# Performance work log

Hardware: AMD Instinct MI355X
Metric: run time of the kernel (lower is better)

## Reference

```python
import jax, jax.numpy as jnp
import numpy as np
from jax import lax

B, N, C_IN, C_OUT = 8, 8192, 64, 128
NUM_SAMPLES, K = 2048, 32
EPS = 1e-5


def _bn(x, g, b, m, v):
    # inference-mode BatchNorm1d over channel axis 1; x: [G, C, L]
    scale = g / jnp.sqrt(v + EPS)
    return (x - m[None, :, None]) * scale[None, :, None] + b[None, :, None]


def _conv1x1(x, w):
    # kernel_size=1 Conv1d (no bias); x: [G, Cin, L], w: [Cout, Cin]
    return jnp.einsum('gck,oc->gok', x, w)


def _res_block(x, w1, g1, b1, m1, v1, w2, g2, b2, m2, v2):
    # conv-bn-relu -> conv-bn, residual add, relu (residual_factor=1.0)
    y = jax.nn.relu(_bn(_conv1x1(x, w1), g1, b1, m1, v1))
    y = _bn(_conv1x1(y, w2), g2, b2, m2, v2)
    return jax.nn.relu(y + x)


def _fps(xyz, num_samples):
    # farthest point sampling; xyz: [B,N,3] -> indices [B,S]
    b, n, _ = xyz.shape

    def step(carry, _):
        dists, last_idx = carry
        last_pt = jnp.take_along_axis(xyz, last_idx[:, None, None], axis=1)  # [B,1,3]
        d = jnp.sum((xyz - last_pt) ** 2, axis=-1)  # [B,N]
        dists = jnp.minimum(dists, d)
        nxt = jnp.argmax(dists, axis=-1).astype(jnp.int32)
        return (dists, nxt), last_idx

    init = (jnp.full((b, n), 1e10, xyz.dtype), jnp.zeros((b,), jnp.int32))
    _, idxs = lax.scan(step, init, None, length=num_samples)
    return jnp.transpose(idxs)  # [B,S]


def setup_inputs():
    key = jax.random.key(0)
    ks = jax.random.split(key, 40)
    xyz = jax.random.uniform(ks[0], (B, N, 3), jnp.float32)
    feat = jax.random.normal(ks[1], (B, N, C_IN), jnp.float32)

    def conv_w(k, o, c):
        return jax.random.normal(k, (o, c), jnp.float32) * (1.0 / np.sqrt(c).astype(np.float32))

    def bn_params(k, c):
        k1, k2, k3, k4 = jax.random.split(k, 4)
        return (1.0 + 0.1 * jax.random.normal(k1, (c,), jnp.float32),
                0.1 * jax.random.normal(k2, (c,), jnp.float32),
                0.1 * jax.random.normal(k3, (c,), jnp.float32),
                jax.random.uniform(k4, (c,), jnp.float32, 0.5, 1.5))

    inp = {'xyz': xyz, 'feat': feat}
    inp['te_w'] = conv_w(ks[2], C_OUT, 2 * C_IN)
    inp['te_g'], inp['te_b'], inp['te_m'], inp['te_v'] = bn_params(ks[3], C_OUT)
    for name, base in (('pre', 4), ('pos', 14)):
        inp[name + '_w1'] = jnp.stack([conv_w(ks[base + i], C_OUT, C_OUT) for i in range(2)])
        inp[name + '_w2'] = jnp.stack([conv_w(ks[base + 2 + i], C_OUT, C_OUT) for i in range(2)])
        bn1 = [bn_params(ks[base + 4 + i], C_OUT) for i in range(2)]
        bn2 = [bn_params(ks[base + 6 + i], C_OUT) for i in range(2)]
        for j, s in enumerate(('g', 'b', 'm', 'v')):
            inp[f'{name}_{s}1'] = jnp.stack([bn1[i][j] for i in range(2)])
            inp[f'{name}_{s}2'] = jnp.stack([bn2[i][j] for i in range(2)])
    return inp


def reference(xyz, feat, te_w, te_g, te_b, te_m, te_v,
              pre_w1, pre_w2, pre_g1, pre_b1, pre_m1, pre_v1, pre_g2, pre_b2, pre_m2, pre_v2,
              pos_w1, pos_w2, pos_g1, pos_b1, pos_m1, pos_v1, pos_g2, pos_b2, pos_m2, pos_v2):
    bsz = xyz.shape[0]
    # --- LocalGrouper: FPS centers + kNN grouping + concat center feat ---
    fps_idx = _fps(xyz, NUM_SAMPLES)                                    # [B,S]
    new_xyz = jnp.take_along_axis(xyz, fps_idx[..., None], axis=1)      # [B,S,3]
    ctr_feat = jnp.take_along_axis(feat, fps_idx[..., None], axis=1)    # [B,S,C]
    d2 = jnp.sum((new_xyz[:, :, None, :] - xyz[:, None, :, :]) ** 2, axis=-1)  # [B,S,N]
    _, knn_idx = lax.top_k(-d2, K)                                      # [B,S,K]
    grouped = feat[jnp.arange(bsz)[:, None, None], knn_idx]             # [B,S,K,C]
    ctr = jnp.broadcast_to(ctr_feat[:, :, None, :], grouped.shape)
    nf = jnp.concatenate([grouped, ctr], axis=-1)                       # [B,S,K,2C]
    # --- permute/view -> [B*S, 2C, K] ---
    x = nf.transpose(0, 1, 3, 2).reshape(bsz * NUM_SAMPLES, 2 * C_IN, K)
    x = jax.nn.relu(_bn(_conv1x1(x, te_w), te_g, te_b, te_m, te_v))     # [G,OUT,K]
    for i in range(2):
        x = _res_block(x, pre_w1[i], pre_g1[i], pre_b1[i], pre_m1[i], pre_v1[i],
                       pre_w2[i], pre_g2[i], pre_b2[i], pre_m2[i], pre_v2[i])
    x = jnp.max(x, axis=-1)                                             # adaptive_max_pool1d(.,1)
    x = x.reshape(bsz, NUM_SAMPLES, C_OUT).transpose(0, 2, 1)           # [B,OUT,S]
    for i in range(2):
        x = _res_block(x, pos_w1[i], pos_g1[i], pos_b1[i], pos_m1[i], pos_v1[i],
                       pos_w2[i], pos_g2[i], pos_b2[i], pos_m2[i], pos_v2[i])
    return new_xyz, x
```

## Files before the change

kernel.cpp:

```cpp
#include <hip/hip_runtime.h>

typedef unsigned short u16;
typedef unsigned int   u32;
typedef unsigned long long u64;

#define B_    8
#define N_    8192
#define CIN   64
#define COUT  128
#define NS    2048
#define K_    32
#define LDSPAD 136

typedef __attribute__((ext_vector_type(8))) short short8;
typedef __attribute__((ext_vector_type(4))) float f32x4;

#define MFMA16(a,b,c) __builtin_amdgcn_mfma_f32_16x16x32_bf16(a,b,c,0,0,0)

__device__ __forceinline__ u16 f2bf(float f){
  u32 u = __float_as_uint(f);
  return (u16)((u + 0x7FFFu + ((u >> 16) & 1u)) >> 16);
}
__device__ __forceinline__ float bf2f(u16 h){ u32 u = ((u32)h) << 16; return __uint_as_float(u); }
__device__ __forceinline__ u32 pack2bf(float lo, float hi){ return (u32)f2bf(lo) | ((u32)f2bf(hi) << 16); }

__global__ void wcvt_kernel(const float* __restrict__ s, u16* __restrict__ d, int n){
  int i = blockIdx.x * 256 + threadIdx.x;
  if (i < n) d[i] = f2bf(s[i]);
}

struct BnPtrs { const float* g[9]; const float* b[9]; const float* m[9]; const float* v[9]; };

__global__ void bn_pre_kernel(BnPtrs p, float* __restrict__ bns){
  int set = blockIdx.x, c = threadIdx.x;
  float sc = p.g[set][c] / sqrtf(p.v[set][c] + 1e-5f);
  bns[set*256 + c]       = sc;
  bns[set*256 + 128 + c] = p.b[set][c] - p.m[set][c] * sc;
}

#define DPP_UMAX(x, ctrl) { \
  u32 o = (u32)__builtin_amdgcn_update_dpp((int)(x), (int)(x), ctrl, 0xf, 0xf, false); \
  x = (o > x) ? o : x; }

__device__ __forceinline__ u32 wave_umax63(u32 x){
  DPP_UMAX(x, 0x111)
  DPP_UMAX(x, 0x112)
  DPP_UMAX(x, 0x114)
  DPP_UMAX(x, 0x118)
  DPP_UMAX(x, 0x142)
  DPP_UMAX(x, 0x143)
  return (u32)__builtin_amdgcn_readlane((int)x, 63);
}

#define FPS_STEP4(j) { \
  f32x4 xv = PX4[j*512 + t]; \
  f32x4 yv = PY4[j*512 + t]; \
  f32x4 zv = PZ4[j*512 + t]; \
  FPS_ONE(j,0) FPS_ONE(j,1) FPS_ONE(j,2) FPS_ONE(j,3) }

#define FPS_ONE(j,i) { \
  float dx = xv[i] - lx; \
  float dy = yv[i] - ly; \
  float dz = zv[i] - lz; \
  float t0 = dx*dx; \
  float t1 = dy*dy; \
  float t2 = dz*dz; \
  float dd = (t0 + t1) + t2;   \
  float nd = fminf(D##j##i, dd); \
  D##j##i = nd; \
  u32 nb = __float_as_uint(nd); \
  tb##j = (nb > tb##j) ? nb : tb##j; }

#define FPS_KMIN(j,i) \
  kk = (__float_as_uint(D##j##i) == wmax && (4*j+i) < kk) ? (4*j+i) : kk;

__global__ __launch_bounds__(512) void fps_kernel(const float* __restrict__ xyz, int* __restrict__ fps_idx){
  #pragma clang fp contract(off)
  const int b = blockIdx.x;
  const int t = threadIdx.x;
  const int lane = t & 63, wv = t >> 6;
  const float* xb = xyz + (size_t)b * N_ * 3;
  __shared__ __align__(16) f32x4 PX4[4*512], PY4[4*512], PZ4[4*512];
  __shared__ u64  kArr[2][8];
  __shared__ float xA[2][8], yA[2][8], zA[2][8];
  const int base = t * 16;
  #pragma unroll
  for (int j = 0; j < 4; ++j){
    f32x4 xv, yv, zv;
    #pragma unroll
    for (int i = 0; i < 4; ++i){
      const int p = base + 4*j + i;
      xv[i] = xb[p*3 + 0];
      yv[i] = xb[p*3 + 1];
      zv[i] = xb[p*3 + 2];
    }
    PX4[j*512 + t] = xv; PY4[j*512 + t] = yv; PZ4[j*512 + t] = zv;
  }
  if (t == 0) fps_idx[b*NS] = 0;
  __syncthreads();
  float D00=1e10f,D01=1e10f,D02=1e10f,D03=1e10f;
  float D10=1e10f,D11=1e10f,D12=1e10f,D13=1e10f;
  float D20=1e10f,D21=1e10f,D22=1e10f,D23=1e10f;
  float D30=1e10f,D31=1e10f,D32=1e10f,D33=1e10f;
  const float* PXs = (const float*)PX4;
  const float* PYs = (const float*)PY4;
  const float* PZs = (const float*)PZ4;
  float lx = PXs[0], ly = PYs[0], lz = PZs[0];
  for (int s = 0; s < NS - 1; ++s){
    u32 tb0 = 0, tb1 = 0, tb2 = 0, tb3 = 0;
    FPS_STEP4(0) FPS_STEP4(1) FPS_STEP4(2) FPS_STEP4(3)
    u32 ta = (tb0 > tb1) ? tb0 : tb1;
    u32 tc = (tb2 > tb3) ? tb2 : tb3;
    u32 tbm = (ta > tc) ? ta : tc;
    const u32 wmax = wave_umax63(tbm);
    const u64 mask = __ballot(tbm == wmax);
    const int fl = __ffsll((long long)mask) - 1;
    const int sl = s & 1;
    if (lane == fl){
      int kk = 64;
      FPS_KMIN(0,0) FPS_KMIN(0,1) FPS_KMIN(0,2) FPS_KMIN(0,3)
      FPS_KMIN(1,0) FPS_KMIN(1,1) FPS_KMIN(1,2) FPS_KMIN(1,3)
      FPS_KMIN(2,0) FPS_KMIN(2,1) FPS_KMIN(2,2) FPS_KMIN(2,3)
      FPS_KMIN(3,0) FPS_KMIN(3,1) FPS_KMIN(3,2) FPS_KMIN(3,3)
      const int pi = base + kk;
      kArr[sl][wv] = ((u64)wmax << 13) | (u64)(8191 - pi);
      const int li = ((kk >> 2)*512 + t)*4 + (kk & 3);
      xA[sl][wv] = PXs[li]; yA[sl][wv] = PYs[li]; zA[sl][wv] = PZs[li];
    }
    __syncthreads();
    u64 win = kArr[sl][0];
    float cx = xA[sl][0], cy = yA[sl][0], cz = zA[sl][0];
    #pragma unroll
    for (int w = 1; w < 8; ++w){
      u64 o = kArr[sl][w];
      float ox = xA[sl][w], oy = yA[sl][w], oz = zA[sl][w];
      bool c = o > win;
      win = c ? o : win; cx = c ? ox : cx; cy = c ? oy : cy; cz = c ? oz : cz;
    }
    lx = cx; ly = cy; lz = cz;
    if (t == 0) fps_idx[b*NS + s + 1] = 8191 - (int)(win & 0x1FFFull);
  }
}

__global__ __launch_bounds__(256) void knn_kernel(const float* __restrict__ xyz, const int* __restrict__ fps_idx,
                                                  int* __restrict__ knn, float* __restrict__ out_xyz){
  #pragma clang fp contract(off)
  const int wid = threadIdx.x >> 6, lane = threadIdx.x & 63;
  const int cg = blockIdx.x * 4 + wid;
  const int b = cg >> 11;
  const float* xb = xyz + (size_t)b * N_ * 3;
  const int ci = fps_idx[cg] & (N_ - 1);
  const float cx = xb[ci*3], cy = xb[ci*3+1], cz = xb[ci*3+2];
  if (lane < 3) out_xyz[cg*3 + lane] = xb[ci*3 + lane];

  float rd = __uint_as_float(0x7F800000u); int ri = 0x7FFFFFFF;
  float r31d = rd; int r31i = ri;
  for (int c = 0; c < N_/64; ++c){
    const int pid = c*64 + lane;
    float dx = xb[pid*3]   - cx;
    float dy = xb[pid*3+1] - cy;
    float dz = xb[pid*3+2] - cz;
    float t0 = dx*dx, t1 = dy*dy, t2 = dz*dz;
    float d2 = (t0 + t1) + t2;
    u64 m = __ballot((d2 < r31d) || (d2 == r31d && pid < r31i));
    while (m){
      int l = __ffsll((long long)m) - 1; m &= m - 1;
      float v = __shfl(d2, l); int vi = c*64 + l;
      if (!((v < r31d) || (v == r31d && vi < r31i))) continue;
      bool lt = (rd < v) || (rd == v && ri < vi);
      int pos = __popcll(__ballot(lt));
      float prd = __shfl_up(rd, 1); int pri = __shfl_up(ri, 1);
      if (lane == pos){ rd = v; ri = vi; }
      else if (lane > pos){ rd = prd; ri = pri; }
      r31d = __shfl(rd, 31); r31i = __shfl(ri, 31);
    }
  }
  if (lane < K_) knn[(size_t)cg * K_ + lane] = ri;
}

__device__ __forceinline__ void zero_acc(f32x4 acc[8][2]){
  #pragma unroll
  for (int mt = 0; mt < 8; ++mt)
    #pragma unroll
    for (int nt = 0; nt < 2; ++nt){
      acc[mt][nt][0] = 0.f; acc[mt][nt][1] = 0.f; acc[mt][nt][2] = 0.f; acc[mt][nt][3] = 0.f;
    }
}

__device__ __forceinline__ void conv_step(const u16* __restrict__ W, const u16* __restrict__ Xw,
                                          int q, int l15, f32x4 acc[8][2]){
  #pragma unroll
  for (int kk = 0; kk < 4; ++kk){
    short8 b0 = *(const short8*)(Xw + l15*LDSPAD + kk*32 + q*8);
    short8 b1 = *(const short8*)(Xw + (16 + l15)*LDSPAD + kk*32 + q*8);
    #pragma unroll
    for (int mt = 0; mt < 8; ++mt){
      short8 a = *(const short8*)(W + (size_t)(mt*16 + l15)*COUT + kk*32 + q*8);
      acc[mt][0] = MFMA16(a, b0, acc[mt][0]);
      acc[mt][1] = MFMA16(a, b1, acc[mt][1]);
    }
  }
}

__device__ __forceinline__ void res_block(const u16* __restrict__ W1, const u16* __restrict__ W2,
    const float* __restrict__ bn1, const float* __restrict__ bn2,
    u16* __restrict__ Xw, int q, int l15, u32 resid[8][2][2], f32x4 acc[8][2], bool writeback){
  zero_acc(acc);
  conv_step(W1, Xw, q, l15, acc);
  #pragma unroll
  for (int mt = 0; mt < 8; ++mt){
    f32x4 sc = *(const f32x4*)(bn1 + mt*16 + q*4);
    f32x4 bi = *(const f32x4*)(bn1 + 128 + mt*16 + q*4);
    #pragma unroll
    for (int nt = 0; nt < 2; ++nt){
      float y0 = fmaxf(fmaf(acc[mt][nt][0], sc[0], bi[0]), 0.f);
      float y1 = fmaxf(fmaf(acc[mt][nt][1], sc[1], bi[1]), 0.f);
      float y2 = fmaxf(fmaf(acc[mt][nt][2], sc[2], bi[2]), 0.f);
      float y3 = fmaxf(fmaf(acc[mt][nt][3], sc[3], bi[3]), 0.f);
      *(uint2*)(Xw + (nt*16 + l15)*LDSPAD + mt*16 + q*4) = make_uint2(pack2bf(y0,y1), pack2bf(y2,y3));
    }
  }
  __syncthreads();
  zero_acc(acc);
  conv_step(W2, Xw, q, l15, acc);
  #pragma unroll
  for (int mt = 0; mt < 8; ++mt){
    f32x4 sc = *(const f32x4*)(bn2 + mt*16 + q*4);
    f32x4 bi = *(const f32x4*)(bn2 + 128 + mt*16 + q*4);
    #pragma unroll
    for (int nt = 0; nt < 2; ++nt){
      float r0 = bf2f((u16)(resid[mt][nt][0] & 0xFFFFu));
      float r1 = bf2f((u16)(resid[mt][nt][0] >> 16));
      float r2 = bf2f((u16)(resid[mt][nt][1] & 0xFFFFu));
      float r3 = bf2f((u16)(resid[mt][nt][1] >> 16));
      float y0 = fmaxf(fmaf(acc[mt][nt][0], sc[0], bi[0]) + r0, 0.f);
      float y1 = fmaxf(fmaf(acc[mt][nt][1], sc[1], bi[1]) + r1, 0.f);
      float y2 = fmaxf(fmaf(acc[mt][nt][2], sc[2], bi[2]) + r2, 0.f);
      float y3 = fmaxf(fmaf(acc[mt][nt][3], sc[3], bi[3]) + r3, 0.f);
      acc[mt][nt][0] = y0; acc[mt][nt][1] = y1; acc[mt][nt][2] = y2; acc[mt][nt][3] = y3;
      if (writeback){
        u32 p0 = pack2bf(y0,y1), p1 = pack2bf(y2,y3);
        resid[mt][nt][0] = p0; resid[mt][nt][1] = p1;
        *(uint2*)(Xw + (nt*16 + l15)*LDSPAD + mt*16 + q*4) = make_uint2(p0, p1);
      }
    }
  }
  if (writeback) __syncthreads();
}

__global__ __launch_bounds__(256) void mid_kernel(const float* __restrict__ feat,
    const u16* __restrict__ te_w, const u16* __restrict__ pre_w1, const u16* __restrict__ pre_w2,
    const float* __restrict__ bns, const int* __restrict__ fps_idx, const int* __restrict__ knn,
    u16* __restrict__ x_mid){
  __shared__ __align__(16) u16 X[4][32*LDSPAD];
  __shared__ __align__(16) float scr[4][128];
  const int wid = threadIdx.x >> 6, lane = threadIdx.x & 63;
  const int q = lane >> 4, l15 = lane & 15;
  const int g = blockIdx.x*4 + wid;
  const int b = g >> 11;
  const float* fb = feat + (size_t)b * N_ * CIN;
  u16* Xw = X[wid];

  const int ctr = fps_idx[g] & (N_ - 1);
  const int* kg = knn + (size_t)g * K_;
  #pragma unroll
  for (int it = 0; it < 4; ++it){
    int lidx = it*64 + lane;
    int col = lidx >> 3, kq = lidx & 7;
    int nb = kg[col] & (N_ - 1);
    f32x4 a0 = *(const f32x4*)(fb + (size_t)nb*CIN + kq*8);
    f32x4 a1 = *(const f32x4*)(fb + (size_t)nb*CIN + kq*8 + 4);
    *(uint2*)(Xw + col*LDSPAD + kq*8)     = make_uint2(pack2bf(a0[0],a0[1]), pack2bf(a0[2],a0[3]));
    *(uint2*)(Xw + col*LDSPAD + kq*8 + 4) = make_uint2(pack2bf(a1[0],a1[1]), pack2bf(a1[2],a1[3]));
    f32x4 c0 = *(const f32x4*)(fb + (size_t)ctr*CIN + kq*8);
    f32x4 c1 = *(const f32x4*)(fb + (size_t)ctr*CIN + kq*8 + 4);
    *(uint2*)(Xw + col*LDSPAD + 64 + kq*8)     = make_uint2(pack2bf(c0[0],c0[1]), pack2bf(c0[2],c0[3]));
    *(uint2*)(Xw + col*LDSPAD + 64 + kq*8 + 4) = make_uint2(pack2bf(c1[0],c1[1]), pack2bf(c1[2],c1[3]));
  }
  __syncthreads();

  f32x4 acc[8][2];
  u32 resid[8][2][2];
  zero_acc(acc);
  conv_step(te_w, Xw, q, l15, acc);
  #pragma unroll
  for (int mt = 0; mt < 8; ++mt){
    f32x4 sc = *(const f32x4*)(bns + mt*16 + q*4);
    f32x4 bi = *(const f32x4*)(bns + 128 + mt*16 + q*4);
    #pragma unroll
    for (int nt = 0; nt < 2; ++nt){
      float y0 = fmaxf(fmaf(acc[mt][nt][0], sc[0], bi[0]), 0.f);
      float y1 = fmaxf(fmaf(acc[mt][nt][1], sc[1], bi[1]), 0.f);
      float y2 = fmaxf(fmaf(acc[mt][nt][2], sc[2], bi[2]), 0.f);
      float y3 = fmaxf(fmaf(acc[mt][nt][3], sc[3], bi[3]), 0.f);
      u32 p0 = pack2bf(y0,y1), p1 = pack2bf(y2,y3);
      resid[mt][nt][0] = p0; resid[mt][nt][1] = p1;
      *(uint2*)(Xw + (nt*16 + l15)*LDSPAD + mt*16 + q*4) = make_uint2(p0, p1);
    }
  }
  __syncthreads();

  res_block(pre_w1,             pre_w2,             bns + 256, bns + 512,  Xw, q, l15, resid, acc, true);
  res_block(pre_w1 + COUT*COUT, pre_w2 + COUT*COUT, bns + 768, bns + 1024, Xw, q, l15, resid, acc, false);

  float mx[8][4];
  #pragma unroll
  for (int mt = 0; mt < 8; ++mt)
    #pragma unroll
    for (int r = 0; r < 4; ++r){
      float m0 = fmaxf(acc[mt][0][r], acc[mt][1][r]);
      #pragma unroll
      for (int off = 1; off < 16; off <<= 1) m0 = fmaxf(m0, __shfl_xor(m0, off));
      mx[mt][r] = m0;
    }
  if (l15 == 0){
    #pragma unroll
    for (int mt = 0; mt < 8; ++mt){
      f32x4 vv; vv[0] = mx[mt][0]; vv[1] = mx[mt][1]; vv[2] = mx[mt][2]; vv[3] = mx[mt][3];
      *(f32x4*)(scr[wid] + mt*16 + q*4) = vv;
    }
  }
  __syncthreads();
  float v0 = scr[wid][lane*2], v1 = scr[wid][lane*2 + 1];
  *(u32*)(x_mid + (size_t)g*COUT + lane*2) = pack2bf(v0, v1);
}

__global__ __launch_bounds__(256) void pos_kernel(const u16* __restrict__ x_mid,
    const u16* __restrict__ pos_w1, const u16* __restrict__ pos_w2,
    const float* __restrict__ bns, float* __restrict__ out_x){
  __shared__ __align__(16) u16 X[4][32*LDSPAD];
  const int wid = threadIdx.x >> 6, lane = threadIdx.x & 63;
  const int q = lane >> 4, l15 = lane & 15;
  const int g = blockIdx.x*4 + wid;
  const int gc0 = g * 32;
  const int b = gc0 >> 11, s0 = gc0 & 2047;
  u16* Xw = X[wid];
  #pragma unroll
  for (int it = 0; it < 8; ++it){
    int lidx = it*64 + lane;
    int col = lidx >> 4, kq = lidx & 15;
    uint4 v = *(const uint4*)(x_mid + (size_t)(gc0 + col)*COUT + kq*8);
    *(uint4*)(Xw + col*LDSPAD + kq*8) = v;
  }
  __syncthreads();
  u32 resid[8][2][2];
  #pragma unroll
  for (int mt = 0; mt < 8; ++mt)
    #pragma unroll
    for (int nt = 0; nt < 2; ++nt){
      uint2 rr = *(const uint2*)(Xw + (nt*16 + l15)*LDSPAD + mt*16 + q*4);
      resid[mt][nt][0] = rr.x; resid[mt][nt][1] = rr.y;
    }
  f32x4 acc[8][2];
  res_block(pos_w1,             pos_w2,             bns + 1280, bns + 1536, Xw, q, l15, resid, acc, true);
  res_block(pos_w1 + COUT*COUT, pos_w2 + COUT*COUT, bns + 1792, bns + 2048, Xw, q, l15, resid, acc, false);
  #pragma unroll
  for (int mt = 0; mt < 8; ++mt)
    #pragma unroll
    for (int nt = 0; nt < 2; ++nt)
      #pragma unroll
      for (int r = 0; r < 4; ++r){
        int row = mt*16 + q*4 + r;
        int colx = s0 + nt*16 + l15;
        out_x[(size_t)(b*COUT + row)*NS + colx] = acc[mt][nt][r];
      }
}

extern "C" void kernel_launch(void* const* d_in, const int* in_sizes, int n_in,
                              void* d_out, int out_size, void* d_ws, size_t ws_size,
                              hipStream_t stream){
  (void)in_sizes; (void)n_in; (void)out_size; (void)ws_size;
  const float* xyz    = (const float*)d_in[0];
  const float* feat   = (const float*)d_in[1];

  char* ws = (char*)d_ws;
  float* bns     = (float*)ws;
  u16*   wbf     = (u16*)(ws + 16384);
  int*   fps_idx = (int*)(ws + 16384 + 294912);
  int*   knn     = (int*)(ws + 16384 + 294912 + 65536);
  u16*   x_mid   = (u16*)(ws + 16384 + 294912 + 65536 + 2097152);
  float* out_xyz = (float*)d_out;
  float* out_x   = (float*)d_out + B_*NS*3;

  u16* te_w   = wbf;
  u16* pre_w1 = wbf + 16384;
  u16* pre_w2 = wbf + 49152;
  u16* pos_w1 = wbf + 81920;
  u16* pos_w2 = wbf + 114688;
  wcvt_kernel<<<64,  256, 0, stream>>>((const float*)d_in[2],  te_w,   16384);
  wcvt_kernel<<<128, 256, 0, stream>>>((const float*)d_in[7],  pre_w1, 32768);
  wcvt_kernel<<<128, 256, 0, stream>>>((const float*)d_in[8],  pre_w2, 32768);
  wcvt_kernel<<<128, 256, 0, stream>>>((const float*)d_in[17], pos_w1, 32768);
  wcvt_kernel<<<128, 256, 0, stream>>>((const float*)d_in[18], pos_w2, 32768);

  BnPtrs bp;
  const int gi[9] = {3, 9, 10, 9, 10, 19, 20, 19, 20};
  const int bbi[9]= {4, 11,12, 11,12, 21, 22, 21, 22};
  const int mi[9] = {5, 13,14, 13,14, 23, 24, 23, 24};
  const int vi[9] = {6, 15,16, 15,16, 25, 26, 25, 26};
  const int of[9] = {0, 0, 0, 128,128, 0, 0, 128,128};
  for (int k = 0; k < 9; ++k){
    bp.g[k] = (const float*)d_in[gi[k]]  + of[k];
    bp.b[k] = (const float*)d_in[bbi[k]] + of[k];
    bp.m[k] = (const float*)d_in[mi[k]]  + of[k];
    bp.v[k] = (const float*)d_in[vi[k]]  + of[k];
  }

  bn_pre_kernel<<<9, 128, 0, stream>>>(bp, bns);
  fps_kernel<<<B_, 512, 0, stream>>>(xyz, fps_idx);
  knn_kernel<<<(B_*NS)/4, 256, 0, stream>>>(xyz, fps_idx, knn, out_xyz);
  mid_kernel<<<(B_*NS)/4, 256, 0, stream>>>(feat, te_w, pre_w1, pre_w2, bns, fps_idx, knn, x_mid);
  pos_kernel<<<(B_*NS/K_)/4, 256, 0, stream>>>(x_mid, pos_w1, pos_w2, bns, out_x);
}
```

Before: 2.965 ms.

## Split FPS across four cooperating blocks per batch with global-memory flag exchange

Farthest point sampling now runs on four blocks per batch, each owning a quarter of the points (4 per thread instead of 16). After each step's in-block reduction, each block publishes its winner to a per-step flag slot in global memory and spin-waits on the other three blocks' slots, then takes the global argmax. The aim is to cut the serial per-step work, since the old version had only 8 blocks doing 16 points per thread. The cost is a cross-block round trip through L2 every step, and correctness depends on all 32 blocks being co-resident. The flag buffer reuses the x_mid workspace and is cleared by an extra kernel.

```diff
diff --git a/kernel.cpp b/kernel.cpp
--- a/kernel.cpp
+++ b/kernel.cpp
@@ -12,6 +12,10 @@
 #define K_    32
 #define LDSPAD 136
 
+#define FPS_NBLK 4
+#define FPS_PPB  (N_/FPS_NBLK)
+#define FPS_PPT  (FPS_PPB/512)
+
 typedef __attribute__((ext_vector_type(8))) short short8;
 typedef __attribute__((ext_vector_type(4))) float f32x4;
 
@@ -27,6 +31,11 @@
 __global__ void wcvt_kernel(const float* __restrict__ s, u16* __restrict__ d, int n){
   int i = blockIdx.x * 256 + threadIdx.x;
   if (i < n) d[i] = f2bf(s[i]);
+}
+
+__global__ void fps_flags_clear_kernel(uint4* __restrict__ p, int n){
+  int i = blockIdx.x * 256 + threadIdx.x;
+  if (i < n) p[i] = make_uint4(0u, 0u, 0u, 0u);
 }
 
 struct BnPtrs { const float* g[9]; const float* b[9]; const float* m[9]; const float* v[9]; };
@@ -52,93 +61,91 @@
   return (u32)__builtin_amdgcn_readlane((int)x, 63);
 }
 
-#define FPS_STEP4(j) { \
-  f32x4 xv = PX4[j*512 + t]; \
-  f32x4 yv = PY4[j*512 + t]; \
-  f32x4 zv = PZ4[j*512 + t]; \
-  FPS_ONE(j,0) FPS_ONE(j,1) FPS_ONE(j,2) FPS_ONE(j,3) }
-
-#define FPS_ONE(j,i) { \
-  float dx = xv[i] - lx; \
-  float dy = yv[i] - ly; \
-  float dz = zv[i] - lz; \
-  float t0 = dx*dx; \
-  float t1 = dy*dy; \
-  float t2 = dz*dz; \
-  float dd = (t0 + t1) + t2;   \
-  float nd = fminf(D##j##i, dd); \
-  D##j##i = nd; \
-  u32 nb = __float_as_uint(nd); \
-  tb##j = (nb > tb##j) ? nb : tb##j; }
-
-#define FPS_KMIN(j,i) \
-  kk = (__float_as_uint(D##j##i) == wmax && (4*j+i) < kk) ? (4*j+i) : kk;
-
-__global__ __launch_bounds__(512) void fps_kernel(const float* __restrict__ xyz, int* __restrict__ fps_idx){
+__global__ __launch_bounds__(512) void fps_kernel(const float* __restrict__ xyz,
+                                                  int* __restrict__ fps_idx,
+                                                  u64* __restrict__ flags){
   #pragma clang fp contract(off)
-  const int b = blockIdx.x;
-  const int t = threadIdx.x;
+  const int bq = blockIdx.x;
+  const int b  = bq & 7;
+  const int q  = bq >> 3;
+  const int t  = threadIdx.x;
   const int lane = t & 63, wv = t >> 6;
   const float* xb = xyz + (size_t)b * N_ * 3;
-  __shared__ __align__(16) f32x4 PX4[4*512], PY4[4*512], PZ4[4*512];
-  __shared__ u64  kArr[2][8];
-  __shared__ float xA[2][8], yA[2][8], zA[2][8];
-  const int base = t * 16;
-  #pragma unroll
-  for (int j = 0; j < 4; ++j){
-    f32x4 xv, yv, zv;
+  __shared__ __align__(16) float PX[N_], PY[N_], PZ[N_];
+  __shared__ u64 kArr[2][8];
+  #pragma unroll
+  for (int i = 0; i < 16; ++i){
+    int p = t*16 + i;
+    PX[p] = xb[p*3 + 0];
+    PY[p] = xb[p*3 + 1];
+    PZ[p] = xb[p*3 + 2];
+  }
+  if (q == 0 && t == 0) fps_idx[b*NS] = 0;
+  __syncthreads();
+
+  const int base = q*FPS_PPB + t*4;
+  const f32x4 px = *(const f32x4*)(PX + base);
+  const f32x4 py = *(const f32x4*)(PY + base);
+  const f32x4 pz = *(const f32x4*)(PZ + base);
+  f32x4 D = {1e10f, 1e10f, 1e10f, 1e10f};
+  float lx = PX[0], ly = PY[0], lz = PZ[0];
+
+  u64* myflag = flags + ((size_t)(b*FPS_NBLK + q)) * NS;
+  u64* nf0 = flags + ((size_t)(b*FPS_NBLK + ((q+1)&3))) * NS;
+  u64* nf1 = flags + ((size_t)(b*FPS_NBLK + ((q+2)&3))) * NS;
+  u64* nf2 = flags + ((size_t)(b*FPS_NBLK + ((q+3)&3))) * NS;
+
+  for (int s = 0; s < NS - 1; ++s){
+    u32 tb = 0;
     #pragma unroll
     for (int i = 0; i < 4; ++i){
-      const int p = base + 4*j + i;
-      xv[i] = xb[p*3 + 0];
-      yv[i] = xb[p*3 + 1];
-      zv[i] = xb[p*3 + 2];
-    }
-    PX4[j*512 + t] = xv; PY4[j*512 + t] = yv; PZ4[j*512 + t] = zv;
-  }
-  if (t == 0) fps_idx[b*NS] = 0;
-  __syncthreads();
-  float D00=1e10f,D01=1e10f,D02=1e10f,D03=1e10f;
-  float D10=1e10f,D11=1e10f,D12=1e10f,D13=1e10f;
-  float D20=1e10f,D21=1e10f,D22=1e10f,D23=1e10f;
-  float D30=1e10f,D31=1e10f,D32=1e10f,D33=1e10f;
-  const float* PXs = (const float*)PX4;
-  const float* PYs = (const float*)PY4;
-  const float* PZs = (const float*)PZ4;
-  float lx = PXs[0], ly = PYs[0], lz = PZs[0];
-  for (int s = 0; s < NS - 1; ++s){
-    u32 tb0 = 0, tb1 = 0, tb2 = 0, tb3 = 0;
-    FPS_STEP4(0) FPS_STEP4(1) FPS_STEP4(2) FPS_STEP4(3)
-    u32 ta = (tb0 > tb1) ? tb0 : tb1;
-    u32 tc = (tb2 > tb3) ? tb2 : tb3;
-    u32 tbm = (ta > tc) ? ta : tc;
-    const u32 wmax = wave_umax63(tbm);
-    const u64 mask = __ballot(tbm == wmax);
+      float dx = px[i] - lx;
+      float dy = py[i] - ly;
+      float dz = pz[i] - lz;
+      float t0 = dx*dx;
+      float t1 = dy*dy;
+      float t2 = dz*dz;
+      float dd = (t0 + t1) + t2;
+      float nd = fminf(D[i], dd);
+      D[i] = nd;
+      u32 nb = __float_as_uint(nd);
+      tb = (nb > tb) ? nb : tb;
+    }
+    const u32 wmax = wave_umax63(tb);
+    const u64 mask = __ballot(tb == wmax);
     const int fl = __ffsll((long long)mask) - 1;
     const int sl = s & 1;
     if (lane == fl){
-      int kk = 64;
-      FPS_KMIN(0,0) FPS_KMIN(0,1) FPS_KMIN(0,2) FPS_KMIN(0,3)
-      FPS_KMIN(1,0) FPS_KMIN(1,1) FPS_KMIN(1,2) FPS_KMIN(1,3)
-      FPS_KMIN(2,0) FPS_KMIN(2,1) FPS_KMIN(2,2) FPS_KMIN(2,3)
-      FPS_KMIN(3,0) FPS_KMIN(3,1) FPS_KMIN(3,2) FPS_KMIN(3,3)
+      int kk = 3;
+      kk = (__float_as_uint(D[2]) == wmax) ? 2 : kk;
+      kk = (__float_as_uint(D[1]) == wmax) ? 1 : kk;
+      kk = (__float_as_uint(D[0]) == wmax) ? 0 : kk;
       const int pi = base + kk;
-      kArr[sl][wv] = ((u64)wmax << 13) | (u64)(8191 - pi);
-      const int li = ((kk >> 2)*512 + t)*4 + (kk & 3);
-      xA[sl][wv] = PXs[li]; yA[sl][wv] = PYs[li]; zA[sl][wv] = PZs[li];
-    }
+      kArr[sl][wv] = (1ull << 63) | ((u64)wmax << 13) | (u64)(8191 - pi);
+    }
+    u64 k0 = __hip_atomic_load(nf0 + s, __ATOMIC_RELAXED, __HIP_MEMORY_SCOPE_AGENT);
+    u64 k1 = __hip_atomic_load(nf1 + s, __ATOMIC_RELAXED, __HIP_MEMORY_SCOPE_AGENT);
+    u64 k2 = __hip_atomic_load(nf2 + s, __ATOMIC_RELAXED, __HIP_MEMORY_SCOPE_AGENT);
     __syncthreads();
     u64 win = kArr[sl][0];
-    float cx = xA[sl][0], cy = yA[sl][0], cz = zA[sl][0];
     #pragma unroll
     for (int w = 1; w < 8; ++w){
       u64 o = kArr[sl][w];
-      float ox = xA[sl][w], oy = yA[sl][w], oz = zA[sl][w];
-      bool c = o > win;
-      win = c ? o : win; cx = c ? ox : cx; cy = c ? oy : cy; cz = c ? oz : cz;
-    }
-    lx = cx; ly = cy; lz = cz;
-    if (t == 0) fps_idx[b*NS + s + 1] = 8191 - (int)(win & 0x1FFFull);
+      win = (o > win) ? o : win;
+    }
+    if (lane == 0)
+      __hip_atomic_store(myflag + s, win, __ATOMIC_RELAXED, __HIP_MEMORY_SCOPE_AGENT);
+    while (!((k0 & k1 & k2) >> 63)){
+      if (!(k0 >> 63)) k0 = __hip_atomic_load(nf0 + s, __ATOMIC_RELAXED, __HIP_MEMORY_SCOPE_AGENT);
+      if (!(k1 >> 63)) k1 = __hip_atomic_load(nf1 + s, __ATOMIC_RELAXED, __HIP_MEMORY_SCOPE_AGENT);
+      if (!(k2 >> 63)) k2 = __hip_atomic_load(nf2 + s, __ATOMIC_RELAXED, __HIP_MEMORY_SCOPE_AGENT);
+    }
+    win = (k0 > win) ? k0 : win;
+    win = (k1 > win) ? k1 : win;
+    win = (k2 > win) ? k2 : win;
+    const int pi = 8191 - (int)(win & 0x1FFFull);
+    lx = PX[pi]; ly = PY[pi]; lz = PZ[pi];
+    if (q == 0 && t == 0) fps_idx[b*NS + s + 1] = pi;
   }
 }
 
@@ -379,6 +386,7 @@
   int*   fps_idx = (int*)(ws + 16384 + 294912);
   int*   knn     = (int*)(ws + 16384 + 294912 + 65536);
   u16*   x_mid   = (u16*)(ws + 16384 + 294912 + 65536 + 2097152);
+  u64*   fflags  = (u64*)x_mid;
   float* out_xyz = (float*)d_out;
   float* out_x   = (float*)d_out + B_*NS*3;
 
@@ -392,6 +400,7 @@
   wcvt_kernel<<<128, 256, 0, stream>>>((const float*)d_in[8],  pre_w2, 32768);
   wcvt_kernel<<<128, 256, 0, stream>>>((const float*)d_in[17], pos_w1, 32768);
   wcvt_kernel<<<128, 256, 0, stream>>>((const float*)d_in[18], pos_w2, 32768);
+  fps_flags_clear_kernel<<<128, 256, 0, stream>>>((uint4*)fflags, (B_*FPS_NBLK*NS*8)/16);
 
   BnPtrs bp;
   const int gi[9] = {3, 9, 10, 9, 10, 19, 20, 19, 20};
@@ -407,7 +416,7 @@
   }
 
   bn_pre_kernel<<<9, 128, 0, stream>>>(bp, bns);
-  fps_kernel<<<B_, 512, 0, stream>>>(xyz, fps_idx);
+  fps_kernel<<<B_*FPS_NBLK, 512, 0, stream>>>(xyz, fps_idx, fflags);
   knn_kernel<<<(B_*NS)/4, 256, 0, stream>>>(xyz, fps_idx, knn, out_xyz);
   mid_kernel<<<(B_*NS)/4, 256, 0, stream>>>(feat, te_w, pre_w1, pre_w2, bns, fps_idx, knn, x_mid);
   pos_kernel<<<(B_*NS/K_)/4, 256, 0, stream>>>(x_mid, pos_w1, pos_w2, bns, out_x);
```

Result: slower. 3.463 ms (+16.8%).

## Fuse FPS, KNN, mid and pos stages into one persistent streaming megakernel

Applied to the files above, without the earlier changes.

Merges the FPS, KNN, grouped-conv mid stage and pos stage into a single launch. Blocks are dispatched by index: the FPS blocks publish each sampled index with release stores, and the KNN/mid waves spin-wait on those entries so neighbour search and convolution overlap the serial FPS loop. The pos waves wait on per-group done flags. KNN indices now stay in registers and are passed by shuffle instead of going through global memory. This depends on the FPS blocks being scheduled first and making progress alongside the spinning blocks, and it raises LDS and register use to a 512-thread block with a shared union.

```diff
diff --git a/kernel.cpp b/kernel.cpp
--- a/kernel.cpp
+++ b/kernel.cpp
@@ -29,6 +29,11 @@
   if (i < n) d[i] = f2bf(s[i]);
 }
 
+__global__ void clear_kernel(int* __restrict__ fps_idx, u32* __restrict__ done){
+  int i = blockIdx.x * 256 + threadIdx.x;
+  if (i < B_*NS){ fps_idx[i] = -1; done[i] = 0u; }
+}
+
 struct BnPtrs { const float* g[9]; const float* b[9]; const float* m[9]; const float* v[9]; };
 
 __global__ void bn_pre_kernel(BnPtrs p, float* __restrict__ bns){
@@ -37,6 +42,22 @@
   bns[set*256 + c]       = sc;
   bns[set*256 + 128 + c] = p.b[set][c] - p.m[set][c] * sc;
 }
+
+struct ShFps {
+  __align__(16) f32x4 PX4[4*512];
+  __align__(16) f32x4 PY4[4*512];
+  __align__(16) f32x4 PZ4[4*512];
+  u64  kArr[2][8];
+  float xA[2][8], yA[2][8], zA[2][8];
+};
+struct ShMid {
+  __align__(16) u16 X[8][32*LDSPAD];
+  __align__(16) float scr[8][128];
+};
+struct ShPos {
+  __align__(16) u16 X[8][32*LDSPAD];
+};
+union ShAll { ShFps f; ShMid m; ShPos p; };
 
 #define DPP_UMAX(x, ctrl) { \
   u32 o = (u32)__builtin_amdgcn_update_dpp((int)(x), (int)(x), ctrl, 0xf, 0xf, false); \
@@ -74,15 +95,12 @@
 #define FPS_KMIN(j,i) \
   kk = (__float_as_uint(D##j##i) == wmax && (4*j+i) < kk) ? (4*j+i) : kk;
 
-__global__ __launch_bounds__(512) void fps_kernel(const float* __restrict__ xyz, int* __restrict__ fps_idx){
+__device__ void fps_path(const float* __restrict__ xyz, int* __restrict__ fps_idx,
+                         ShFps& S, int b, int t){
   #pragma clang fp contract(off)
-  const int b = blockIdx.x;
-  const int t = threadIdx.x;
   const int lane = t & 63, wv = t >> 6;
   const float* xb = xyz + (size_t)b * N_ * 3;
-  __shared__ __align__(16) f32x4 PX4[4*512], PY4[4*512], PZ4[4*512];
-  __shared__ u64  kArr[2][8];
-  __shared__ float xA[2][8], yA[2][8], zA[2][8];
+  f32x4* PX4 = S.PX4; f32x4* PY4 = S.PY4; f32x4* PZ4 = S.PZ4;
   const int base = t * 16;
   #pragma unroll
   for (int j = 0; j < 4; ++j){
@@ -96,7 +114,8 @@
     }
     PX4[j*512 + t] = xv; PY4[j*512 + t] = yv; PZ4[j*512 + t] = zv;
   }
-  if (t == 0) fps_idx[b*NS] = 0;
+  if (t == 0)
+    __hip_atomic_store(fps_idx + b*NS, 0, __ATOMIC_RELEASE, __HIP_MEMORY_SCOPE_AGENT);
   __syncthreads();
   float D00=1e10f,D01=1e10f,D02=1e10f,D03=1e10f;
   float D10=1e10f,D11=1e10f,D12=1e10f,D13=1e10f;
@@ -123,35 +142,115 @@
       FPS_KMIN(2,0) FPS_KMIN(2,1) FPS_KMIN(2,2) FPS_KMIN(2,3)
       FPS_KMIN(3,0) FPS_KMIN(3,1) FPS_KMIN(3,2) FPS_KMIN(3,3)
       const int pi = base + kk;
-      kArr[sl][wv] = ((u64)wmax << 13) | (u64)(8191 - pi);
+      S.kArr[sl][wv] = ((u64)wmax << 13) | (u64)(8191 - pi);
       const int li = ((kk >> 2)*512 + t)*4 + (kk & 3);
-      xA[sl][wv] = PXs[li]; yA[sl][wv] = PYs[li]; zA[sl][wv] = PZs[li];
+      S.xA[sl][wv] = PXs[li]; S.yA[sl][wv] = PYs[li]; S.zA[sl][wv] = PZs[li];
     }
     __syncthreads();
-    u64 win = kArr[sl][0];
-    float cx = xA[sl][0], cy = yA[sl][0], cz = zA[sl][0];
+    u64 win = S.kArr[sl][0];
+    float cx = S.xA[sl][0], cy = S.yA[sl][0], cz = S.zA[sl][0];
     #pragma unroll
     for (int w = 1; w < 8; ++w){
-      u64 o = kArr[sl][w];
-      float ox = xA[sl][w], oy = yA[sl][w], oz = zA[sl][w];
+      u64 o = S.kArr[sl][w];
+      float ox = S.xA[sl][w], oy = S.yA[sl][w], oz = S.zA[sl][w];
       bool c = o > win;
       win = c ? o : win; cx = c ? ox : cx; cy = c ? oy : cy; cz = c ? oz : cz;
     }
     lx = cx; ly = cy; lz = cz;
-    if (t == 0) fps_idx[b*NS + s + 1] = 8191 - (int)(win & 0x1FFFull);
-  }
-}
-
-__global__ __launch_bounds__(256) void knn_kernel(const float* __restrict__ xyz, const int* __restrict__ fps_idx,
-                                                  int* __restrict__ knn, float* __restrict__ out_xyz){
+    if (t == 0)
+      __hip_atomic_store(fps_idx + b*NS + s + 1, 8191 - (int)(win & 0x1FFFull),
+                         __ATOMIC_RELEASE, __HIP_MEMORY_SCOPE_AGENT);
+  }
+}
+
+__device__ __forceinline__ void zero_acc(f32x4 acc[8][2]){
+  #pragma unroll
+  for (int mt = 0; mt < 8; ++mt)
+    #pragma unroll
+    for (int nt = 0; nt < 2; ++nt){
+      acc[mt][nt][0] = 0.f; acc[mt][nt][1] = 0.f; acc[mt][nt][2] = 0.f; acc[mt][nt][3] = 0.f;
+    }
+}
+
+__device__ __forceinline__ void conv_step(const u16* __restrict__ W, const u16* __restrict__ Xw,
+                                          int q, int l15, f32x4 acc[8][2]){
+  #pragma unroll
+  for (int kk = 0; kk < 4; ++kk){
+    short8 b0 = *(const short8*)(Xw + l15*LDSPAD + kk*32 + q*8);
+    short8 b1 = *(const short8*)(Xw + (16 + l15)*LDSPAD + kk*32 + q*8);
+    #pragma unroll
+    for (int mt = 0; mt < 8; ++mt){
+      short8 a = *(const short8*)(W + (size_t)(mt*16 + l15)*COUT + kk*32 + q*8);
+      acc[mt][0] = MFMA16(a, b0, acc[mt][0]);
+      acc[mt][1] = MFMA16(a, b1, acc[mt][1]);
+    }
+  }
+}
+
+__device__ __forceinline__ void res_block(const u16* __restrict__ W1, const u16* __restrict__ W2,
+    const float* __restrict__ bn1, const float* __restrict__ bn2,
+    u16* __restrict__ Xw, int q, int l15, u32 resid[8][2][2], f32x4 acc[8][2], bool writeback){
+  zero_acc(acc);
+  conv_step(W1, Xw, q, l15, acc);
+  #pragma unroll
+  for (int mt = 0; mt < 8; ++mt){
+    f32x4 sc = *(const f32x4*)(bn1 + mt*16 + q*4);
+    f32x4 bi = *(const f32x4*)(bn1 + 128 + mt*16 + q*4);
+    #pragma unroll
+    for (int nt = 0; nt < 2; ++nt){
+      float y0 = fmaxf(fmaf(acc[mt][nt][0], sc[0], bi[0]), 0.f);
+      float y1 = fmaxf(fmaf(acc[mt][nt][1], sc[1], bi[1]), 0.f);
+      float y2 = fmaxf(fmaf(acc[mt][nt][2], sc[2], bi[2]), 0.f);
+      float y3 = fmaxf(fmaf(acc[mt][nt][3], sc[3], bi[3]), 0.f);
+      *(uint2*)(Xw + (nt*16 + l15)*LDSPAD + mt*16 + q*4) = make_uint2(pack2bf(y0,y1), pack2bf(y2,y3));
+    }
+  }
+  __syncthreads();
+  zero_acc(acc);
+  conv_step(W2, Xw, q, l15, acc);
+  #pragma unroll
+  for (int mt = 0; mt < 8; ++mt){
+    f32x4 sc = *(const f32x4*)(bn2 + mt*16 + q*4);
+    f32x4 bi = *(const f32x4*)(bn2 + 128 + mt*16 + q*4);
+    #pragma unroll
+    for (int nt = 0; nt < 2; ++nt){
+      float r0 = bf2f((u16)(resid[mt][nt][0] & 0xFFFFu));
+      float r1 = bf2f((u16)(resid[mt][nt][0] >> 16));
+      float r2 = bf2f((u16)(resid[mt][nt][1] & 0xFFFFu));
+      float r3 = bf2f((u16)(resid[mt][nt][1] >> 16));
+      float y0 = fmaxf(fmaf(acc[mt][nt][0], sc[0], bi[0]) + r0, 0.f);
+      float y1 = fmaxf(fmaf(acc[mt][nt][1], sc[1], bi[1]) + r1, 0.f);
+      float y2 = fmaxf(fmaf(acc[mt][nt][2], sc[2], bi[2]) + r2, 0.f);
+      float y3 = fmaxf(fmaf(acc[mt][nt][3], sc[3], bi[3]) + r3, 0.f);
+      acc[mt][nt][0] = y0; acc[mt][nt][1] = y1; acc[mt][nt][2] = y2; acc[mt][nt][3] = y3;
+      if (writeback){
+        u32 p0 = pack2bf(y0,y1), p1 = pack2bf(y2,y3);
+        resid[mt][nt][0] = p0; resid[mt][nt][1] = p1;
+        *(uint2*)(Xw + (nt*16 + l15)*LDSPAD + mt*16 + q*4) = make_uint2(p0, p1);
+      }
+    }
+  }
+  if (writeback) __syncthreads();
+}
+
+__device__ void knnmid_path(const float* __restrict__ xyz, const float* __restrict__ feat,
+    const u16* __restrict__ te_w, const u16* __restrict__ pre_w1, const u16* __restrict__ pre_w2,
+    const float* __restrict__ bns, int* __restrict__ fps_idx,
+    u16* __restrict__ x_mid, u32* __restrict__ done, float* __restrict__ out_xyz,
+    u16* __restrict__ Xw, float* __restrict__ scrw, int g, int lane){
   #pragma clang fp contract(off)
-  const int wid = threadIdx.x >> 6, lane = threadIdx.x & 63;
-  const int cg = blockIdx.x * 4 + wid;
-  const int b = cg >> 11;
+  const int b = g >> 11;
   const float* xb = xyz + (size_t)b * N_ * 3;
-  const int ci = fps_idx[cg] & (N_ - 1);
+
+  int raw;
+  for (;;){
+    raw = __hip_atomic_load(fps_idx + g, __ATOMIC_RELAXED, __HIP_MEMORY_SCOPE_AGENT);
+    if (raw >= 0) break;
+    __builtin_amdgcn_s_sleep(4);
+  }
+  const int ci = raw & (N_ - 1);
   const float cx = xb[ci*3], cy = xb[ci*3+1], cz = xb[ci*3+2];
-  if (lane < 3) out_xyz[cg*3 + lane] = xb[ci*3 + lane];
+  if (lane < 3) out_xyz[g*3 + lane] = xb[ci*3 + lane];
 
   float rd = __uint_as_float(0x7F800000u); int ri = 0x7FFFFFFF;
   float r31d = rd; int r31i = ri;
@@ -175,105 +274,21 @@
       r31d = __shfl(rd, 31); r31i = __shfl(ri, 31);
     }
   }
-  if (lane < K_) knn[(size_t)cg * K_ + lane] = ri;
-}
-
-__device__ __forceinline__ void zero_acc(f32x4 acc[8][2]){
-  #pragma unroll
-  for (int mt = 0; mt < 8; ++mt)
-    #pragma unroll
-    for (int nt = 0; nt < 2; ++nt){
-      acc[mt][nt][0] = 0.f; acc[mt][nt][1] = 0.f; acc[mt][nt][2] = 0.f; acc[mt][nt][3] = 0.f;
-    }
-}
-
-__device__ __forceinline__ void conv_step(const u16* __restrict__ W, const u16* __restrict__ Xw,
-                                          int q, int l15, f32x4 acc[8][2]){
-  #pragma unroll
-  for (int kk = 0; kk < 4; ++kk){
-    short8 b0 = *(const short8*)(Xw + l15*LDSPAD + kk*32 + q*8);
-    short8 b1 = *(const short8*)(Xw + (16 + l15)*LDSPAD + kk*32 + q*8);
-    #pragma unroll
-    for (int mt = 0; mt < 8; ++mt){
-      short8 a = *(const short8*)(W + (size_t)(mt*16 + l15)*COUT + kk*32 + q*8);
-      acc[mt][0] = MFMA16(a, b0, acc[mt][0]);
-      acc[mt][1] = MFMA16(a, b1, acc[mt][1]);
-    }
-  }
-}
-
-__device__ __forceinline__ void res_block(const u16* __restrict__ W1, const u16* __restrict__ W2,
-    const float* __restrict__ bn1, const float* __restrict__ bn2,
-    u16* __restrict__ Xw, int q, int l15, u32 resid[8][2][2], f32x4 acc[8][2], bool writeback){
-  zero_acc(acc);
-  conv_step(W1, Xw, q, l15, acc);
-  #pragma unroll
-  for (int mt = 0; mt < 8; ++mt){
-    f32x4 sc = *(const f32x4*)(bn1 + mt*16 + q*4);
-    f32x4 bi = *(const f32x4*)(bn1 + 128 + mt*16 + q*4);
-    #pragma unroll
-    for (int nt = 0; nt < 2; ++nt){
-      float y0 = fmaxf(fmaf(acc[mt][nt][0], sc[0], bi[0]), 0.f);
-      float y1 = fmaxf(fmaf(acc[mt][nt][1], sc[1], bi[1]), 0.f);
-      float y2 = fmaxf(fmaf(acc[mt][nt][2], sc[2], bi[2]), 0.f);
-      float y3 = fmaxf(fmaf(acc[mt][nt][3], sc[3], bi[3]), 0.f);
-      *(uint2*)(Xw + (nt*16 + l15)*LDSPAD + mt*16 + q*4) = make_uint2(pack2bf(y0,y1), pack2bf(y2,y3));
-    }
-  }
-  __syncthreads();
-  zero_acc(acc);
-  conv_step(W2, Xw, q, l15, acc);
-  #pragma unroll
-  for (int mt = 0; mt < 8; ++mt){
-    f32x4 sc = *(const f32x4*)(bn2 + mt*16 + q*4);
-    f32x4 bi = *(const f32x4*)(bn2 + 128 + mt*16 + q*4);
-    #pragma unroll
-    for (int nt = 0; nt < 2; ++nt){
-      float r0 = bf2f((u16)(resid[mt][nt][0] & 0xFFFFu));
-      float r1 = bf2f((u16)(resid[mt][nt][0] >> 16));
-      float r2 = bf2f((u16)(resid[mt][nt][1] & 0xFFFFu));
-      float r3 = bf2f((u16)(resid[mt][nt][1] >> 16));
-      float y0 = fmaxf(fmaf(acc[mt][nt][0], sc[0], bi[0]) + r0, 0.f);
-      float y1 = fmaxf(fmaf(acc[mt][nt][1], sc[1], bi[1]) + r1, 0.f);
-      float y2 = fmaxf(fmaf(acc[mt][nt][2], sc[2], bi[2]) + r2, 0.f);
-      float y3 = fmaxf(fmaf(acc[mt][nt][3], sc[3], bi[3]) + r3, 0.f);
-      acc[mt][nt][0] = y0; acc[mt][nt][1] = y1; acc[mt][nt][2] = y2; acc[mt][nt][3] = y3;
-      if (writeback){
-        u32 p0 = pack2bf(y0,y1), p1 = pack2bf(y2,y3);
-        resid[mt][nt][0] = p0; resid[mt][nt][1] = p1;
-        *(uint2*)(Xw + (nt*16 + l15)*LDSPAD + mt*16 + q*4) = make_uint2(p0, p1);
-      }
-    }
-  }
-  if (writeback) __syncthreads();
-}
-
-__global__ __launch_bounds__(256) void mid_kernel(const float* __restrict__ feat,
-    const u16* __restrict__ te_w, const u16* __restrict__ pre_w1, const u16* __restrict__ pre_w2,
-    const float* __restrict__ bns, const int* __restrict__ fps_idx, const int* __restrict__ knn,
-    u16* __restrict__ x_mid){
-  __shared__ __align__(16) u16 X[4][32*LDSPAD];
-  __shared__ __align__(16) float scr[4][128];
-  const int wid = threadIdx.x >> 6, lane = threadIdx.x & 63;
+
   const int q = lane >> 4, l15 = lane & 15;
-  const int g = blockIdx.x*4 + wid;
-  const int b = g >> 11;
   const float* fb = feat + (size_t)b * N_ * CIN;
-  u16* Xw = X[wid];
-
-  const int ctr = fps_idx[g] & (N_ - 1);
-  const int* kg = knn + (size_t)g * K_;
   #pragma unroll
   for (int it = 0; it < 4; ++it){
     int lidx = it*64 + lane;
-    int col = lidx >> 3, kq = lidx & 7;
-    int nb = kg[col] & (N_ - 1);
+    int kq = lidx & 7;
+    int col = it*8 + (lane >> 3);
+    int nb = __shfl(ri, col) & (N_ - 1);
     f32x4 a0 = *(const f32x4*)(fb + (size_t)nb*CIN + kq*8);
     f32x4 a1 = *(const f32x4*)(fb + (size_t)nb*CIN + kq*8 + 4);
     *(uint2*)(Xw + col*LDSPAD + kq*8)     = make_uint2(pack2bf(a0[0],a0[1]), pack2bf(a0[2],a0[3]));
     *(uint2*)(Xw + col*LDSPAD + kq*8 + 4) = make_uint2(pack2bf(a1[0],a1[1]), pack2bf(a1[2],a1[3]));
-    f32x4 c0 = *(const f32x4*)(fb + (size_t)ctr*CIN + kq*8);
-    f32x4 c1 = *(const f32x4*)(fb + (size_t)ctr*CIN + kq*8 + 4);
+    f32x4 c0 = *(const f32x4*)(fb + (size_t)ci*CIN + kq*8);
+    f32x4 c1 = *(const f32x4*)(fb + (size_t)ci*CIN + kq*8 + 4);
     *(uint2*)(Xw + col*LDSPAD + 64 + kq*8)     = make_uint2(pack2bf(c0[0],c0[1]), pack2bf(c0[2],c0[3]));
     *(uint2*)(Xw + col*LDSPAD + 64 + kq*8 + 4) = make_uint2(pack2bf(c1[0],c1[1]), pack2bf(c1[2],c1[3]));
   }
@@ -317,24 +332,31 @@
     #pragma unroll
     for (int mt = 0; mt < 8; ++mt){
       f32x4 vv; vv[0] = mx[mt][0]; vv[1] = mx[mt][1]; vv[2] = mx[mt][2]; vv[3] = mx[mt][3];
-      *(f32x4*)(scr[wid] + mt*16 + q*4) = vv;
-    }
-  }
-  __syncthreads();
-  float v0 = scr[wid][lane*2], v1 = scr[wid][lane*2 + 1];
+      *(f32x4*)(scrw + mt*16 + q*4) = vv;
+    }
+  }
+  __syncthreads();
+  float v0 = scrw[lane*2], v1 = scrw[lane*2 + 1];
   *(u32*)(x_mid + (size_t)g*COUT + lane*2) = pack2bf(v0, v1);
-}
-
-__global__ __launch_bounds__(256) void pos_kernel(const u16* __restrict__ x_mid,
+  if (lane == 0)
+    __hip_atomic_store(done + g, 1u, __ATOMIC_RELEASE, __HIP_MEMORY_SCOPE_AGENT);
+}
+
+__device__ void pos_path(const u16* __restrict__ x_mid,
     const u16* __restrict__ pos_w1, const u16* __restrict__ pos_w2,
-    const float* __restrict__ bns, float* __restrict__ out_x){
-  __shared__ __align__(16) u16 X[4][32*LDSPAD];
-  const int wid = threadIdx.x >> 6, lane = threadIdx.x & 63;
+    const float* __restrict__ bns, float* __restrict__ out_x,
+    u32* __restrict__ done, u16* __restrict__ Xw, int g, int lane){
   const int q = lane >> 4, l15 = lane & 15;
-  const int g = blockIdx.x*4 + wid;
   const int gc0 = g * 32;
   const int b = gc0 >> 11, s0 = gc0 & 2047;
-  u16* Xw = X[wid];
+  for (;;){
+    u32 d = (lane < 32)
+      ? __hip_atomic_load(done + gc0 + lane, __ATOMIC_RELAXED, __HIP_MEMORY_SCOPE_AGENT)
+      : 1u;
+    if (__all(d != 0)) break;
+    __builtin_amdgcn_s_sleep(4);
+  }
+  __builtin_amdgcn_fence(__ATOMIC_ACQUIRE, "agent");
   #pragma unroll
   for (int it = 0; it < 8; ++it){
     int lidx = it*64 + lane;
@@ -366,6 +388,33 @@
       }
 }
 
+#define GRID_FPS    B_
+#define GRID_KM     (B_*NS/8)
+#define GRID_POS    (B_*NS/K_/8)
+
+__global__ __launch_bounds__(512) void mega_kernel(
+    const float* __restrict__ xyz, const float* __restrict__ feat,
+    const u16* __restrict__ te_w, const u16* __restrict__ pre_w1, const u16* __restrict__ pre_w2,
+    const u16* __restrict__ pos_w1, const u16* __restrict__ pos_w2,
+    const float* __restrict__ bns, int* __restrict__ fps_idx,
+    u16* __restrict__ x_mid, u32* __restrict__ done,
+    float* __restrict__ out_xyz, float* __restrict__ out_x){
+  __shared__ ShAll sh;
+  const int bid = blockIdx.x;
+  const int t = threadIdx.x;
+  const int wid = t >> 6, lane = t & 63;
+  if (bid < GRID_FPS){
+    fps_path(xyz, fps_idx, sh.f, bid, t);
+  } else if (bid < GRID_FPS + GRID_KM){
+    const int g = (bid - GRID_FPS)*8 + wid;
+    knnmid_path(xyz, feat, te_w, pre_w1, pre_w2, bns, fps_idx, x_mid, done, out_xyz,
+                sh.m.X[wid], sh.m.scr[wid], g, lane);
+  } else {
+    const int g = (bid - GRID_FPS - GRID_KM)*8 + wid;
+    pos_path(x_mid, pos_w1, pos_w2, bns, out_x, done, sh.p.X[wid], g, lane);
+  }
+}
+
 extern "C" void kernel_launch(void* const* d_in, const int* in_sizes, int n_in,
                               void* d_out, int out_size, void* d_ws, size_t ws_size,
                               hipStream_t stream){
@@ -377,8 +426,8 @@
   float* bns     = (float*)ws;
   u16*   wbf     = (u16*)(ws + 16384);
   int*   fps_idx = (int*)(ws + 16384 + 294912);
-  int*   knn     = (int*)(ws + 16384 + 294912 + 65536);
-  u16*   x_mid   = (u16*)(ws + 16384 + 294912 + 65536 + 2097152);
+  u32*   done    = (u32*)(ws + 16384 + 294912 + 65536);
+  u16*   x_mid   = (u16*)(ws + 16384 + 294912 + 65536 + 65536);
   float* out_xyz = (float*)d_out;
   float* out_x   = (float*)d_out + B_*NS*3;
 
@@ -392,6 +441,7 @@
   wcvt_kernel<<<128, 256, 0, stream>>>((const float*)d_in[8],  pre_w2, 32768);
   wcvt_kernel<<<128, 256, 0, stream>>>((const float*)d_in[17], pos_w1, 32768);
   wcvt_kernel<<<128, 256, 0, stream>>>((const float*)d_in[18], pos_w2, 32768);
+  clear_kernel<<<64, 256, 0, stream>>>(fps_idx, done);
 
   BnPtrs bp;
   const int gi[9] = {3, 9, 10, 9, 10, 19, 20, 19, 20};
@@ -407,8 +457,7 @@
   }
 
   bn_pre_kernel<<<9, 128, 0, stream>>>(bp, bns);
-  fps_kernel<<<B_, 512, 0, stream>>>(xyz, fps_idx);
-  knn_kernel<<<(B_*NS)/4, 256, 0, stream>>>(xyz, fps_idx, knn, out_xyz);
-  mid_kernel<<<(B_*NS)/4, 256, 0, stream>>>(feat, te_w, pre_w1, pre_w2, bns, fps_idx, knn, x_mid);
-  pos_kernel<<<(B_*NS/K_)/4, 256, 0, stream>>>(x_mid, pos_w1, pos_w2, bns, out_x);
-}
+  mega_kernel<<<GRID_FPS + GRID_KM + GRID_POS, 512, 0, stream>>>(
+      xyz, feat, te_w, pre_w1, pre_w2, pos_w1, pos_w2, bns,
+      fps_idx, x_mid, done, out_xyz, out_x);
+}
```

New measurement: 3.196 ms. 1.08x slower.
